# Kernel tuning notes

Measured on AMD Instinct MI355X. Metric: run time of the kernel, lower is better.

Reference implementation:

```python
import jax, jax.numpy as jnp
import numpy as np

N = 100000   # num_nodes
E = 1600000  # num_edges (avg degree 16)
D = 128      # in_channels
H = 128      # hidden_channels
P = 0.1      # dropout prob
NEG_SLOPE = 0.01  # F.leaky_relu default


def setup_inputs() -> dict:
    key = jax.random.key(0)
    k0, k1, k2, k3 = jax.random.split(key, 4)
    x = jax.random.normal(k0, (N, D), jnp.float32)
    edge_index = jax.random.randint(k1, (2, E), 0, N, dtype=jnp.int64)
    # GCNConv: lin = Linear(in, out, bias=False) (glorot), plus additive bias after aggregation
    W1 = jax.random.normal(k2, (D, H), jnp.float32) / np.float32(np.sqrt(D))
    b1 = jnp.zeros((H,), jnp.float32)
    W2 = jax.random.normal(k3, (H, H), jnp.float32) / np.float32(np.sqrt(H))
    b2 = jnp.zeros((H,), jnp.float32)
    return {"x": x, "edge_index": edge_index, "W1": W1, "b1": b1, "W2": W2, "b2": b2}


def _gcn_conv(x, W, b, src, dst, deg_inv_sqrt):
    # PyG GCNConv: h = x @ W; symmetric norm with self-loops; scatter-add to dst; + bias
    h = x @ W                                             # [N, H]
    norm = deg_inv_sqrt[src] * deg_inv_sqrt[dst]          # [E]
    agg = jax.ops.segment_sum(h[src] * norm[:, None], dst, num_segments=N)
    agg = agg + h * (deg_inv_sqrt * deg_inv_sqrt)[:, None]  # self-loop term (norm = 1/deg)
    return agg + b


def reference(x, edge_index, W1, b1, W2, b2):
    src, dst = edge_index[0], edge_index[1]
    # degree with self-loops (gcn_norm: deg computed over col = dst)
    deg = jax.ops.segment_sum(jnp.ones((E,), x.dtype), dst, num_segments=N) + 1.0
    deg_inv_sqrt = jax.lax.rsqrt(deg)

    h = _gcn_conv(x, W1, b1, src, dst, deg_inv_sqrt)
    h = jax.nn.leaky_relu(h, NEG_SLOPE)
    # deterministic dropout mask (training-mode dropout with fixed key)
    keep = jax.random.bernoulli(jax.random.key(42), 1.0 - P, h.shape)
    h = jnp.where(keep, h / (1.0 - P), 0.0)

    return _gcn_conv(h, W2, b2, src, dst, deg_inv_sqrt)
```

## Files before the change

### kernel.cpp

```cpp
#include <hip/hip_runtime.h>
#include <cstdint>


#define CH 128

__device__ __forceinline__ uint32_t rotl32(uint32_t v, int r) {
  return (v << r) | (v >> (32 - r));
}

__device__ __forceinline__ void threefry2x32(uint32_t k0, uint32_t k1,
                                             uint32_t x0, uint32_t x1,
                                             uint32_t& o0, uint32_t& o1) {
  const uint32_t ks2 = k0 ^ k1 ^ 0x1BD11BDAu;
  x0 += k0; x1 += k1;
  x0 += x1; x1 = rotl32(x1, 13); x1 ^= x0;
  x0 += x1; x1 = rotl32(x1, 15); x1 ^= x0;
  x0 += x1; x1 = rotl32(x1, 26); x1 ^= x0;
  x0 += x1; x1 = rotl32(x1,  6); x1 ^= x0;
  x0 += k1; x1 += ks2 + 1u;
  x0 += x1; x1 = rotl32(x1, 17); x1 ^= x0;
  x0 += x1; x1 = rotl32(x1, 29); x1 ^= x0;
  x0 += x1; x1 = rotl32(x1, 16); x1 ^= x0;
  x0 += x1; x1 = rotl32(x1, 24); x1 ^= x0;
  x0 += ks2; x1 += k0 + 2u;
  x0 += x1; x1 = rotl32(x1, 13); x1 ^= x0;
  x0 += x1; x1 = rotl32(x1, 15); x1 ^= x0;
  x0 += x1; x1 = rotl32(x1, 26); x1 ^= x0;
  x0 += x1; x1 = rotl32(x1,  6); x1 ^= x0;
  x0 += k0; x1 += k1 + 3u;
  x0 += x1; x1 = rotl32(x1, 17); x1 ^= x0;
  x0 += x1; x1 = rotl32(x1, 29); x1 ^= x0;
  x0 += x1; x1 = rotl32(x1, 16); x1 ^= x0;
  x0 += x1; x1 = rotl32(x1, 24); x1 ^= x0;
  x0 += k1; x1 += ks2 + 4u;
  x0 += x1; x1 = rotl32(x1, 13); x1 ^= x0;
  x0 += x1; x1 = rotl32(x1, 15); x1 ^= x0;
  x0 += x1; x1 = rotl32(x1, 26); x1 ^= x0;
  x0 += x1; x1 = rotl32(x1,  6); x1 ^= x0;
  x0 += ks2; x1 += k0 + 5u;
  o0 = x0; o1 = x1;
}

__device__ __forceinline__ bool keep_mask(uint32_t i) {
  uint32_t o0, o1;
  threefry2x32(0u, 42u, 0u, i, o0, o1);
  const uint32_t bits = o0 ^ o1;
  float u = __uint_as_float((bits >> 9) | 0x3f800000u) - 1.0f;
  return u < 0.9f;
}

__global__ void k_hist(const int* __restrict__ ei, int* __restrict__ cnt, int E) {
  int e = blockIdx.x * blockDim.x + threadIdx.x;
  if (e < E) {
    int dst = ei[E + e];
    atomicAdd(&cnt[dst], 1);
  }
}

__global__ __launch_bounds__(256) void k_scan1(const int* __restrict__ cnt,
                                               int* __restrict__ bsum, int n) {
  const int tid = threadIdx.x;
  const int i0 = blockIdx.x * 1024 + tid * 4;
  int s = 0;
  if (i0 + 3 < n) {
    int4 v = *reinterpret_cast<const int4*>(&cnt[i0]);
    s = v.x + v.y + v.z + v.w;
  } else {
    for (int k = 0; k < 4; ++k) if (i0 + k < n) s += cnt[i0 + k];
  }
  __shared__ int red[256];
  red[tid] = s;
  __syncthreads();
  for (int d = 128; d > 0; d >>= 1) {
    if (tid < d) red[tid] += red[tid + d];
    __syncthreads();
  }
  if (tid == 0) bsum[blockIdx.x] = red[0];
}

__global__ __launch_bounds__(128) void k_scan2(const int* __restrict__ bsum,
                                               int* __restrict__ bpre, int nb) {
  __shared__ int sh[128];
  const int t = threadIdx.x;
  int carry = 0;
  for (int base = 0; base < nb; base += 128) {
    int v = (base + t < nb) ? bsum[base + t] : 0;
    sh[t] = v;
    __syncthreads();
    for (int d = 1; d < 128; d <<= 1) {
      int u = (t >= d) ? sh[t - d] : 0;
      __syncthreads();
      sh[t] += u;
      __syncthreads();
    }
    if (base + t < nb) bpre[base + t] = carry + sh[t] - v;
    carry += sh[127];
    __syncthreads();
  }
}

__global__ __launch_bounds__(256) void k_scan3(const int* __restrict__ cnt,
                                               const int* __restrict__ bpre,
                                               int* __restrict__ offs,
                                               int* __restrict__ cursor,
                                               float* __restrict__ dis,
                                               int n, int Etot) {
  const int tid = threadIdx.x;
  const int i0 = blockIdx.x * 1024 + tid * 4;
  int c0 = 0, c1 = 0, c2 = 0, c3 = 0;
  if (i0 + 3 < n) {
    int4 v = *reinterpret_cast<const int4*>(&cnt[i0]);
    c0 = v.x; c1 = v.y; c2 = v.z; c3 = v.w;
  } else {
    if (i0 + 0 < n) c0 = cnt[i0 + 0];
    if (i0 + 1 < n) c1 = cnt[i0 + 1];
    if (i0 + 2 < n) c2 = cnt[i0 + 2];
    if (i0 + 3 < n) c3 = cnt[i0 + 3];
  }
  const int s = c0 + c1 + c2 + c3;
  __shared__ int sh[256];
  sh[tid] = s;
  __syncthreads();
  for (int d = 1; d < 256; d <<= 1) {
    int u = (tid >= d) ? sh[tid - d] : 0;
    __syncthreads();
    sh[tid] += u;
    __syncthreads();
  }
  int pre = bpre[blockIdx.x] + sh[tid] - s;
  int cc[4] = {c0, c1, c2, c3};
  #pragma unroll
  for (int k = 0; k < 4; ++k) {
    int i = i0 + k;
    if (i < n) {
      offs[i] = pre;
      cursor[i] = pre;
      dis[i] = rsqrtf((float)cc[k] + 1.0f);
      pre += cc[k];
    }
  }
  if (blockIdx.x == 0 && tid == 0) offs[n] = Etot;
}

__global__ void k_scatter(const int* __restrict__ ei, int* __restrict__ cursor,
                          int* __restrict__ csr, int E) {
  int e = blockIdx.x * blockDim.x + threadIdx.x;
  if (e < E) {
    int src = ei[e];
    int dst = ei[E + e];
    int p = atomicAdd(&cursor[dst], 1);
    csr[p] = src;
  }
}

__global__ __launch_bounds__(256) void k_gemm(const float* __restrict__ A,
                                              const float* __restrict__ B,
                                              float* __restrict__ C, int M) {
  __shared__ float As[64][132];
  __shared__ float Bs[128][68];
  const int tid = threadIdx.x;
  const int rowBase = blockIdx.x * 64;
  const int colBase = blockIdx.y * 64;

  #pragma unroll
  for (int i = 0; i < 8; ++i) {
    int f = tid + i * 256;
    int r = f >> 5;
    int c4 = (f & 31) << 2;
    int gr = rowBase + r;
    float4 v = make_float4(0.f, 0.f, 0.f, 0.f);
    if (gr < M) v = *reinterpret_cast<const float4*>(&A[(size_t)gr * CH + c4]);
    As[r][c4 + 0] = v.x; As[r][c4 + 1] = v.y; As[r][c4 + 2] = v.z; As[r][c4 + 3] = v.w;
  }
  #pragma unroll
  for (int i = 0; i < 8; ++i) {
    int f = tid + i * 256;
    int r = f >> 4;
    int c4 = (f & 15) << 2;
    float4 v = *reinterpret_cast<const float4*>(&B[r * CH + colBase + c4]);
    Bs[r][c4 + 0] = v.x; Bs[r][c4 + 1] = v.y; Bs[r][c4 + 2] = v.z; Bs[r][c4 + 3] = v.w;
  }
  __syncthreads();

  const int tx = tid & 15, ty = tid >> 4;
  const int r0 = ty * 4, c0 = tx * 4;
  float acc[4][4] = {};
  #pragma unroll 4
  for (int k = 0; k < 128; ++k) {
    float a0 = As[r0 + 0][k], a1 = As[r0 + 1][k], a2 = As[r0 + 2][k], a3 = As[r0 + 3][k];
    float4 b = *reinterpret_cast<const float4*>(&Bs[k][c0]);
    acc[0][0] += a0 * b.x; acc[0][1] += a0 * b.y; acc[0][2] += a0 * b.z; acc[0][3] += a0 * b.w;
    acc[1][0] += a1 * b.x; acc[1][1] += a1 * b.y; acc[1][2] += a1 * b.z; acc[1][3] += a1 * b.w;
    acc[2][0] += a2 * b.x; acc[2][1] += a2 * b.y; acc[2][2] += a2 * b.z; acc[2][3] += a2 * b.w;
    acc[3][0] += a3 * b.x; acc[3][1] += a3 * b.y; acc[3][2] += a3 * b.z; acc[3][3] += a3 * b.w;
  }
  #pragma unroll
  for (int i = 0; i < 4; ++i) {
    int gr = rowBase + r0 + i;
    if (gr < M) {
      float4 v = make_float4(acc[i][0], acc[i][1], acc[i][2], acc[i][3]);
      *reinterpret_cast<float4*>(&C[(size_t)gr * CH + colBase + c0]) = v;
    }
  }
}

template <int LAYER>
__global__ __launch_bounds__(256) void k_agg(const float* __restrict__ H,
                                             const int* __restrict__ offs,
                                             const int* __restrict__ csr,
                                             const float* __restrict__ dis,
                                             const float* __restrict__ bias,
                                             float* __restrict__ out, int n) {
  int wid = (blockIdx.x * 256 + threadIdx.x) >> 6;
  int lane = threadIdx.x & 63;
  if (wid >= n) return;
  const int row = wid;
  const float dd = dis[row];
  int e = offs[row];
  const int end = offs[row + 1];
  const int c = lane * 2;
  float ax0 = 0.f, ay0 = 0.f, ax1 = 0.f, ay1 = 0.f;
  for (; e + 1 < end; e += 2) {
    int s0 = csr[e], s1 = csr[e + 1];
    float n0 = dis[s0] * dd, n1 = dis[s1] * dd;
    float2 v0 = *reinterpret_cast<const float2*>(&H[(size_t)s0 * CH + c]);
    float2 v1 = *reinterpret_cast<const float2*>(&H[(size_t)s1 * CH + c]);
    ax0 += v0.x * n0; ay0 += v0.y * n0;
    ax1 += v1.x * n1; ay1 += v1.y * n1;
  }
  if (e < end) {
    int s0 = csr[e];
    float n0 = dis[s0] * dd;
    float2 v0 = *reinterpret_cast<const float2*>(&H[(size_t)s0 * CH + c]);
    ax0 += v0.x * n0; ay0 += v0.y * n0;
  }
  float2 vs = *reinterpret_cast<const float2*>(&H[(size_t)row * CH + c]);
  float ax = ax0 + ax1 + vs.x * dd * dd + bias[c];
  float ay = ay0 + ay1 + vs.y * dd * dd + bias[c + 1];
  if (LAYER == 1) {
    ax = ax > 0.f ? ax : 0.01f * ax;
    ay = ay > 0.f ? ay : 0.01f * ay;
    uint32_t i0 = (uint32_t)row * (uint32_t)CH + (uint32_t)c;
    ax = keep_mask(i0)      ? ax * (1.0f / 0.9f) : 0.0f;
    ay = keep_mask(i0 + 1u) ? ay * (1.0f / 0.9f) : 0.0f;
  }
  float2 o; o.x = ax; o.y = ay;
  *reinterpret_cast<float2*>(&out[(size_t)row * CH + c]) = o;
}

extern "C" void kernel_launch(void* const* d_in, const int* in_sizes, int n_in,
                              void* d_out, int out_size, void* d_ws, size_t ws_size,
                              hipStream_t stream) {
  const float* x = (const float*)d_in[0];
  const int* ei = (const int*)d_in[1];
  const float* W1 = (const float*)d_in[2];
  const float* b1 = (const float*)d_in[3];
  const float* W2 = (const float*)d_in[4];
  const float* b2 = (const float*)d_in[5];
  float* out = (float*)d_out;

  const int N = in_sizes[0] / CH;
  const int E = in_sizes[1] / 2;
  const int nb = (N + 1023) / 1024;

  char* ws = (char*)d_ws;
  size_t o = 0;
  auto take = [&](size_t bytes) -> void* {
    void* p = ws + o;
    o = (o + bytes + 255) & ~(size_t)255;
    return p;
  };
  int* cnt    = (int*)take((size_t)N * 4);
  int* offs   = (int*)take((size_t)(N + 1) * 4);
  int* cursor = (int*)take((size_t)N * 4);
  float* dis  = (float*)take((size_t)N * 4);
  int* csr    = (int*)take((size_t)E * 4);
  int* bsum   = (int*)take((size_t)nb * 4);
  int* bpre   = (int*)take((size_t)nb * 4);
  float* Hws  = (float*)take((size_t)N * CH * 4);

  hipMemsetAsync(cnt, 0, (size_t)N * 4, stream);

  const int eb = (E + 255) / 256;
  k_hist<<<eb, 256, 0, stream>>>(ei, cnt, E);
  k_scan1<<<nb, 256, 0, stream>>>(cnt, bsum, N);
  k_scan2<<<1, 128, 0, stream>>>(bsum, bpre, nb);
  k_scan3<<<nb, 256, 0, stream>>>(cnt, bpre, offs, cursor, dis, N, E);
  k_scatter<<<eb, 256, 0, stream>>>(ei, cursor, csr, E);

  dim3 gg((N + 63) / 64, CH / 64);
  const int ab = (N + 3) / 4;
  k_gemm<<<gg, 256, 0, stream>>>(x, W1, Hws, N);
  k_agg<1><<<ab, 256, 0, stream>>>(Hws, offs, csr, dis, b1, out, N);
  k_gemm<<<gg, 256, 0, stream>>>(out, W2, Hws, N);
  k_agg<2><<<ab, 256, 0, stream>>>(Hws, offs, csr, dis, b2, out, N);
}
```

Measured before the change: 700.2 us.

## Fold source-degree normalization into GEMM epilogue and unroll aggregation by four

```diff
diff --git a/kernel.cpp b/kernel.cpp
--- a/kernel.cpp
+++ b/kernel.cpp
@@ -155,6 +155,7 @@
 
 __global__ __launch_bounds__(256) void k_gemm(const float* __restrict__ A,
                                               const float* __restrict__ B,
+                                              const float* __restrict__ rs,
                                               float* __restrict__ C, int M) {
   __shared__ float As[64][132];
   __shared__ float Bs[128][68];
@@ -198,7 +199,9 @@
   for (int i = 0; i < 4; ++i) {
     int gr = rowBase + r0 + i;
     if (gr < M) {
-      float4 v = make_float4(acc[i][0], acc[i][1], acc[i][2], acc[i][3]);
+      const float s = rs[gr];
+      float4 v = make_float4(acc[i][0] * s, acc[i][1] * s,
+                             acc[i][2] * s, acc[i][3] * s);
       *reinterpret_cast<float4*>(&C[(size_t)gr * CH + colBase + c0]) = v;
     }
   }
@@ -220,23 +223,26 @@
   const int end = offs[row + 1];
   const int c = lane * 2;
   float ax0 = 0.f, ay0 = 0.f, ax1 = 0.f, ay1 = 0.f;
-  for (; e + 1 < end; e += 2) {
-    int s0 = csr[e], s1 = csr[e + 1];
-    float n0 = dis[s0] * dd, n1 = dis[s1] * dd;
+  float ax2 = 0.f, ay2 = 0.f, ax3 = 0.f, ay3 = 0.f;
+  for (; e + 3 < end; e += 4) {
+    int s0 = csr[e], s1 = csr[e + 1], s2 = csr[e + 2], s3 = csr[e + 3];
     float2 v0 = *reinterpret_cast<const float2*>(&H[(size_t)s0 * CH + c]);
     float2 v1 = *reinterpret_cast<const float2*>(&H[(size_t)s1 * CH + c]);
-    ax0 += v0.x * n0; ay0 += v0.y * n0;
-    ax1 += v1.x * n1; ay1 += v1.y * n1;
-  }
-  if (e < end) {
+    float2 v2 = *reinterpret_cast<const float2*>(&H[(size_t)s2 * CH + c]);
+    float2 v3 = *reinterpret_cast<const float2*>(&H[(size_t)s3 * CH + c]);
+    ax0 += v0.x; ay0 += v0.y;
+    ax1 += v1.x; ay1 += v1.y;
+    ax2 += v2.x; ay2 += v2.y;
+    ax3 += v3.x; ay3 += v3.y;
+  }
+  for (; e < end; ++e) {
     int s0 = csr[e];
-    float n0 = dis[s0] * dd;
     float2 v0 = *reinterpret_cast<const float2*>(&H[(size_t)s0 * CH + c]);
-    ax0 += v0.x * n0; ay0 += v0.y * n0;
+    ax0 += v0.x; ay0 += v0.y;
   }
   float2 vs = *reinterpret_cast<const float2*>(&H[(size_t)row * CH + c]);
-  float ax = ax0 + ax1 + vs.x * dd * dd + bias[c];
-  float ay = ay0 + ay1 + vs.y * dd * dd + bias[c + 1];
+  float ax = ((ax0 + ax1) + (ax2 + ax3) + vs.x) * dd + bias[c];
+  float ay = ((ay0 + ay1) + (ay2 + ay3) + vs.y) * dd + bias[c + 1];
   if (LAYER == 1) {
     ax = ax > 0.f ? ax : 0.01f * ax;
     ay = ay > 0.f ? ay : 0.01f * ay;
@@ -290,8 +296,8 @@
 
   dim3 gg((N + 63) / 64, CH / 64);
   const int ab = (N + 3) / 4;
-  k_gemm<<<gg, 256, 0, stream>>>(x, W1, Hws, N);
+  k_gemm<<<gg, 256, 0, stream>>>(x, W1, dis, Hws, N);
   k_agg<1><<<ab, 256, 0, stream>>>(Hws, offs, csr, dis, b1, out, N);
-  k_gemm<<<gg, 256, 0, stream>>>(out, W2, Hws, N);
+  k_gemm<<<gg, 256, 0, stream>>>(out, W2, dis, Hws, N);
   k_agg<2><<<ab, 256, 0, stream>>>(Hws, offs, csr, dis, b2, out, N);
 }
```

Result: faster. 663.3 us (-5.3%).
